# Kernel tuning notes

Hardware: AMD Instinct MI355X
Metric: run time of the kernel (lower is better)

The kernel has to match this reference:

```python
import jax, jax.numpy as jnp
import numpy as np

B, A, EH, DH, H, W = 32, 512, 256, 384, 64, 64  # batch, attn_size, enc_hs, dec_hs, spatial


def setup_inputs() -> dict:
    key = jax.random.key(0)
    ks = jax.random.split(key, 5)
    return {
        "dec_h": jax.random.normal(ks[0], (B, DH), jnp.float32),
        "weighted_enc_out": jax.random.normal(ks[1], (B, A, H, W), jnp.float32),
        "enc_out": jax.random.normal(ks[2], (B, EH, H, W), jnp.float32),
        # decoder_linear: Linear(dec_hs -> attn_size)
        "W_dec": jax.random.normal(ks[3], (A, DH), jnp.float32) / np.sqrt(DH).astype(np.float32),
        "b_dec": jnp.zeros((A,), jnp.float32),
        # energy_layer: Conv2d(attn_size -> 1, kernel 1x1) == per-pixel dot with a vector
        "w_energy": jax.random.normal(ks[4], (A,), jnp.float32) / np.sqrt(A).astype(np.float32),
        "b_energy": jnp.zeros((), jnp.float32),
    }


def reference(dec_h, weighted_enc_out, enc_out, W_dec, b_dec, w_energy, b_energy):
    # decoder_linear(dec_h): [B, DH] -> [B, A]
    dec_proj = dec_h @ W_dec.T + b_dec
    # broadcast add over spatial dims + tanh: [B, A, H, W]
    pre_scores = jnp.tanh(weighted_enc_out + dec_proj[:, :, None, None])
    # 1x1 conv to 1 channel == contraction over channel axis: [B, H, W]
    scores = jnp.einsum('bahw,a->bhw', pre_scores, w_energy) + b_energy
    # softmax over flattened spatial dims
    b, h, w = scores.shape
    alphas = jax.nn.softmax(scores.reshape(b, h * w), axis=1).reshape(b, h, w)
    # weighted sum of encoder features: [B, EH]
    context = jnp.einsum('bchw,bhw->bc', enc_out, alphas)
    return context, alphas
```

## Files before the change

### kernel.cpp

```cpp
#include <hip/hip_runtime.h>
#include <math.h>

#define B  32
#define A  512
#define EH 256
#define DH 384
#define HW 4096
#define NCHUNK 8
#define ACH (A / NCHUNK)
#define P4 (HW / 4)

typedef float f4 __attribute__((ext_vector_type(4)));

__global__ void k_scores_part(const float* __restrict__ weo,
                              const float* __restrict__ dec_h,
                              const float* __restrict__ W_dec,
                              const float* __restrict__ b_dec,
                              const float* __restrict__ w_energy,
                              float* __restrict__ partial) {
    __shared__ float s_dp[ACH];
    __shared__ float s_we[ACH];
    const int b  = blockIdx.z;
    const int a0 = blockIdx.y * ACH;
    const int p4 = blockIdx.x * blockDim.x + threadIdx.x;
    const float C = 2.8853900817779268f;

    const int wave = threadIdx.x >> 6;
    const int lane = threadIdx.x & 63;
    const float* dh = dec_h + b * DH;
    #pragma unroll
    for (int i = 0; i < 16; i += 2) {
        const int a1 = wave * 16 + i;
        const int a2 = a1 + 1;
        const float* wd1 = W_dec + (size_t)(a0 + a1) * DH;
        const float* wd2 = W_dec + (size_t)(a0 + a2) * DH;
        float acc1 = 0.f, acc2 = 0.f;
        #pragma unroll
        for (int k = 0; k < DH; k += 64) {
            float d = dh[k + lane];
            acc1 = fmaf(d, wd1[k + lane], acc1);
            acc2 = fmaf(d, wd2[k + lane], acc2);
        }
        #pragma unroll
        for (int s = 32; s > 0; s >>= 1) {
            acc1 += __shfl_down(acc1, s);
            acc2 += __shfl_down(acc2, s);
        }
        if (lane == 0) {
            s_dp[a1] = (acc1 + b_dec[a0 + a1]) * C;
            s_dp[a2] = (acc2 + b_dec[a0 + a2]) * C;
        }
    }
    if (threadIdx.x < ACH) s_we[threadIdx.x] = w_energy[a0 + threadIdx.x];
    __syncthreads();

    const f4* w4 = (const f4*)(weo + ((size_t)b * A + a0) * HW);
    f4 acc = (f4)(0.f);
    #pragma unroll 8
    for (int a = 0; a < ACH; ++a) {
        f4 x = __builtin_nontemporal_load(&w4[(size_t)a * P4 + p4]);
        float dp = s_dp[a];
        float we = s_we[a];
        float rx = __builtin_amdgcn_rcpf(__builtin_amdgcn_exp2f(fmaf(x.x, C, dp)) + 1.f);
        float ry = __builtin_amdgcn_rcpf(__builtin_amdgcn_exp2f(fmaf(x.y, C, dp)) + 1.f);
        float rz = __builtin_amdgcn_rcpf(__builtin_amdgcn_exp2f(fmaf(x.z, C, dp)) + 1.f);
        float rw = __builtin_amdgcn_rcpf(__builtin_amdgcn_exp2f(fmaf(x.w, C, dp)) + 1.f);
        acc.x = fmaf(we, fmaf(-2.f, rx, 1.f), acc.x);
        acc.y = fmaf(we, fmaf(-2.f, ry, 1.f), acc.y);
        acc.z = fmaf(we, fmaf(-2.f, rz, 1.f), acc.z);
        acc.w = fmaf(we, fmaf(-2.f, rw, 1.f), acc.w);
    }
    f4* out4 = (f4*)partial;
    __builtin_nontemporal_store(acc, &out4[((size_t)(b * NCHUNK + blockIdx.y)) * P4 + p4]);
}

__global__ void k_softmax(const float* __restrict__ partial,
                          const float* __restrict__ b_energy,
                          float* __restrict__ alphas) {
    __shared__ float red[256];
    const int b = blockIdx.x;
    const float be = b_energy[0];
    const float4* p4 = (const float4*)partial + (size_t)b * NCHUNK * P4;
    float4 v[4];
    float m = -INFINITY;
    #pragma unroll
    for (int i = 0; i < 4; ++i) {
        const int idx = threadIdx.x + i * 256;
        float4 s = make_float4(be, be, be, be);
        #pragma unroll
        for (int c = 0; c < NCHUNK; ++c) {
            float4 t = p4[(size_t)c * P4 + idx];
            s.x += t.x; s.y += t.y; s.z += t.z; s.w += t.w;
        }
        v[i] = s;
        m = fmaxf(m, fmaxf(fmaxf(s.x, s.y), fmaxf(s.z, s.w)));
    }
    red[threadIdx.x] = m; __syncthreads();
    for (int s2 = 128; s2 > 0; s2 >>= 1) {
        if (threadIdx.x < s2)
            red[threadIdx.x] = fmaxf(red[threadIdx.x], red[threadIdx.x + s2]);
        __syncthreads();
    }
    m = red[0]; __syncthreads();
    float sum = 0.f;
    #pragma unroll
    for (int i = 0; i < 4; ++i) {
        v[i].x = __expf(v[i].x - m); v[i].y = __expf(v[i].y - m);
        v[i].z = __expf(v[i].z - m); v[i].w = __expf(v[i].w - m);
        sum += v[i].x + v[i].y + v[i].z + v[i].w;
    }
    red[threadIdx.x] = sum; __syncthreads();
    for (int s2 = 128; s2 > 0; s2 >>= 1) {
        if (threadIdx.x < s2)
            red[threadIdx.x] += red[threadIdx.x + s2];
        __syncthreads();
    }
    const float inv = 1.f / red[0];
    float4* out = (float4*)(alphas + (size_t)b * HW);
    #pragma unroll
    for (int i = 0; i < 4; ++i)
        out[threadIdx.x + i * 256] =
            make_float4(v[i].x * inv, v[i].y * inv, v[i].z * inv, v[i].w * inv);
}

__global__ void k_context(const float* __restrict__ enc,
                          const float* __restrict__ alphas,
                          float* __restrict__ context) {
    __shared__ float4 s_al[P4];
    const int b = blockIdx.y;
    const float4* a4 = (const float4*)(alphas + (size_t)b * HW);
    #pragma unroll
    for (int i = 0; i < 4; ++i)
        s_al[threadIdx.x + i * 256] = a4[threadIdx.x + i * 256];
    __syncthreads();

    const int wave = threadIdx.x >> 6;
    const int lane = threadIdx.x & 63;
    const int c = blockIdx.x * 4 + wave;
    const f4* e4 = (const f4*)(enc + ((size_t)b * EH + c) * HW);
    float acc = 0.f;
    #pragma unroll
    for (int it = 0; it < 16; ++it) {
        f4 v = __builtin_nontemporal_load(&e4[it * 64 + lane]);
        float4 al = s_al[it * 64 + lane];
        acc = fmaf(v.x, al.x, fmaf(v.y, al.y, fmaf(v.z, al.z, fmaf(v.w, al.w, acc))));
    }
    #pragma unroll
    for (int s = 32; s > 0; s >>= 1)
        acc += __shfl_down(acc, s);
    if (lane == 0) context[b * EH + c] = acc;
}

extern "C" void kernel_launch(void* const* d_in, const int* in_sizes, int n_in,
                              void* d_out, int out_size, void* d_ws, size_t ws_size,
                              hipStream_t stream) {
    const float* dec_h = (const float*)d_in[0];
    const float* weo   = (const float*)d_in[1];
    const float* enc   = (const float*)d_in[2];
    const float* W_dec = (const float*)d_in[3];
    const float* b_dec = (const float*)d_in[4];
    const float* w_en  = (const float*)d_in[5];
    const float* b_en  = (const float*)d_in[6];

    float* context = (float*)d_out;
    float* alphas  = context + B * EH;

    float* partial = (float*)d_ws;

    k_scores_part<<<dim3(P4 / 256, NCHUNK, B), 256, 0, stream>>>(
        weo, dec_h, W_dec, b_dec, w_en, partial);
    k_softmax<<<dim3(B), 256, 0, stream>>>(partial, b_en, alphas);
    k_context<<<dim3(EH / 4, B), 256, 0, stream>>>(enc, alphas, context);
}
```

Baseline: 429.6 us.

## Fuse softmax into context kernel, recomputing softmax per block

Merges the softmax and context kernels into one launch. Each of 16 blocks per batch recomputes the softmax from the partial scores and keeps alphas in shared memory, and block 0 also writes alphas out. This drops one kernel launch and the global round trip of alphas. In exchange the 128 KB partial buffer per batch is read 16 times. The partial-score store also changes from nontemporal to a normal cached store, likely so those repeated reads can hit in cache.

```diff
diff --git a/kernel.cpp b/kernel.cpp
--- a/kernel.cpp
+++ b/kernel.cpp
@@ -70,17 +70,22 @@
         acc.z = fmaf(we, fmaf(-2.f, rz, 1.f), acc.z);
         acc.w = fmaf(we, fmaf(-2.f, rw, 1.f), acc.w);
     }
-    f4* out4 = (f4*)partial;
-    __builtin_nontemporal_store(acc, &out4[((size_t)(b * NCHUNK + blockIdx.y)) * P4 + p4]);
+    float4* out4 = (float4*)partial;
+    out4[((size_t)(b * NCHUNK + blockIdx.y)) * P4 + p4] =
+        make_float4(acc.x, acc.y, acc.z, acc.w);
 }
 
-__global__ void k_softmax(const float* __restrict__ partial,
-                          const float* __restrict__ b_energy,
-                          float* __restrict__ alphas) {
+__global__ void k_ctx_softmax(const float* __restrict__ partial,
+                              const float* __restrict__ enc,
+                              const float* __restrict__ b_energy,
+                              float* __restrict__ alphas,
+                              float* __restrict__ context) {
+    __shared__ float4 s_al[P4];
     __shared__ float red[256];
-    const int b = blockIdx.x;
+    const int b = blockIdx.y;
     const float be = b_energy[0];
     const float4* p4 = (const float4*)partial + (size_t)b * NCHUNK * P4;
+
     float4 v[4];
     float m = -INFINITY;
     #pragma unroll
@@ -116,39 +121,39 @@
         __syncthreads();
     }
     const float inv = 1.f / red[0];
-    float4* out = (float4*)(alphas + (size_t)b * HW);
     #pragma unroll
-    for (int i = 0; i < 4; ++i)
-        out[threadIdx.x + i * 256] =
-            make_float4(v[i].x * inv, v[i].y * inv, v[i].z * inv, v[i].w * inv);
-}
-
-__global__ void k_context(const float* __restrict__ enc,
-                          const float* __restrict__ alphas,
-                          float* __restrict__ context) {
-    __shared__ float4 s_al[P4];
-    const int b = blockIdx.y;
-    const float4* a4 = (const float4*)(alphas + (size_t)b * HW);
-    #pragma unroll
-    for (int i = 0; i < 4; ++i)
-        s_al[threadIdx.x + i * 256] = a4[threadIdx.x + i * 256];
+    for (int i = 0; i < 4; ++i) {
+        const int idx = threadIdx.x + i * 256;
+        s_al[idx] = make_float4(v[i].x * inv, v[i].y * inv, v[i].z * inv, v[i].w * inv);
+    }
+    if (blockIdx.x == 0) {
+        float4* out = (float4*)(alphas + (size_t)b * HW);
+        #pragma unroll
+        for (int i = 0; i < 4; ++i) {
+            const int idx = threadIdx.x + i * 256;
+            out[idx] = make_float4(v[i].x * inv, v[i].y * inv, v[i].z * inv, v[i].w * inv);
+        }
+    }
     __syncthreads();
 
     const int wave = threadIdx.x >> 6;
     const int lane = threadIdx.x & 63;
-    const int c = blockIdx.x * 4 + wave;
-    const f4* e4 = (const f4*)(enc + ((size_t)b * EH + c) * HW);
-    float acc = 0.f;
     #pragma unroll
-    for (int it = 0; it < 16; ++it) {
-        f4 v = __builtin_nontemporal_load(&e4[it * 64 + lane]);
-        float4 al = s_al[it * 64 + lane];
-        acc = fmaf(v.x, al.x, fmaf(v.y, al.y, fmaf(v.z, al.z, fmaf(v.w, al.w, acc))));
+    for (int i = 0; i < 4; ++i) {
+        const int c = blockIdx.x * 16 + wave * 4 + i;
+        const f4* e4 = (const f4*)(enc + ((size_t)b * EH + c) * HW);
+        float acc = 0.f;
+        #pragma unroll
+        for (int it = 0; it < 16; ++it) {
+            f4 ev = __builtin_nontemporal_load(&e4[it * 64 + lane]);
+            float4 al = s_al[it * 64 + lane];
+            acc = fmaf(ev.x, al.x, fmaf(ev.y, al.y, fmaf(ev.z, al.z, fmaf(ev.w, al.w, acc))));
+        }
+        #pragma unroll
+        for (int s = 32; s > 0; s >>= 1)
+            acc += __shfl_down(acc, s);
+        if (lane == 0) context[(size_t)b * EH + c] = acc;
     }
-    #pragma unroll
-    for (int s = 32; s > 0; s >>= 1)
-        acc += __shfl_down(acc, s);
-    if (lane == 0) context[b * EH + c] = acc;
 }
 
 extern "C" void kernel_launch(void* const* d_in, const int* in_sizes, int n_in,
@@ -169,6 +174,5 @@
 
     k_scores_part<<<dim3(P4 / 256, NCHUNK, B), 256, 0, stream>>>(
         weo, dec_h, W_dec, b_dec, w_en, partial);
-    k_softmax<<<dim3(B), 256, 0, stream>>>(partial, b_en, alphas);
-    k_context<<<dim3(EH / 4, B), 256, 0, stream>>>(enc, alphas, context);
+    k_ctx_softmax<<<dim3(16, B), 256, 0, stream>>>(partial, enc, b_en, alphas, context);
 }
```

Result: no change. 432.2 us (+0.6%).
